# Optimization experiments

Hardware: AMD Instinct MI355X
Metric: run time of the kernel (lower is better)

The kernel has to match this reference:

```python
import jax, jax.numpy as jnp
import numpy as np

TOP_K = 2

def setup_inputs() -> dict:
    key = jax.random.key(0)
    k1, k2 = jax.random.split(key)
    B, S, D, E = 4, 8192, 1024, 64
    hidden_states = jax.random.normal(k1, (B, S, D), dtype=jnp.float32)
    gate_weight = jax.random.normal(k2, (E, D), dtype=jnp.float32) * (1.0 / D ** 0.5)
    return {"hidden_states": hidden_states, "gate_weight": gate_weight}

def reference(hidden_states, gate_weight):
    # router_logits: [B, S, E] = hidden @ W^T
    router_logits = jnp.einsum('bsd,ed->bse', hidden_states, gate_weight)
    # softmax in float32 (matches .float() in torch), cast back to input dtype
    router_probs = jax.nn.softmax(router_logits.astype(jnp.float32), axis=-1).astype(hidden_states.dtype)
    top_k_probs, selected_experts = jax.lax.top_k(router_probs, TOP_K)
    top_k_probs = top_k_probs / (jnp.sum(top_k_probs, axis=-1, keepdims=True) + 1e-08)
    return top_k_probs, selected_experts, router_logits
```

## Files before the change

### kernel.cpp

```cpp
#include <hip/hip_runtime.h>
#include <math.h>


typedef __attribute__((ext_vector_type(8))) short bf16x8;
typedef __attribute__((ext_vector_type(4))) float f32x4;

static constexpr int TOKENS = 32768;
static constexpr int DDIM   = 1024;
static constexpr int NEXP   = 64;
static constexpr size_t OFF_EXP = 65536;
static constexpr size_t OFF_LOG = 131072;

__global__ void w_split3_kernel(const float* __restrict__ w,
                                short* __restrict__ w1,
                                short* __restrict__ w2,
                                short* __restrict__ w3) {
    int idx = blockIdx.x * blockDim.x + threadIdx.x;
    for (int i = idx; i < NEXP * DDIM; i += gridDim.x * blockDim.x) {
        int e = i >> 10, k = i & 1023;
        float f = w[i];
        unsigned u1 = __float_as_uint(f);
        float f1 = __uint_as_float(u1 & 0xffff0000u);
        float r1 = f - f1;
        unsigned u2 = __float_as_uint(r1);
        float f2 = __uint_as_float(u2 & 0xffff0000u);
        float r2 = r1 - f2;
        unsigned u3 = __float_as_uint(r2);
        int n = e >> 4, c = k >> 5;
        int lane = (e & 15) + ((k & 31) >> 3) * 16;
        int j = k & 7;
        size_t dst = ((size_t)(c * 4 + n) * 64 + lane) * 8 + j;
        w1[dst] = (short)(u1 >> 16);
        w2[dst] = (short)(u2 >> 16);
        w3[dst] = (short)(u3 >> 16);
    }
}

__device__ inline void split8(float4 a, float4 b,
                              bf16x8& o1, bf16x8& o2, bf16x8& o3) {
    float f[8] = {a.x, a.y, a.z, a.w, b.x, b.y, b.z, b.w};
#pragma unroll
    for (int j = 0; j < 8; ++j) {
        unsigned u1 = __float_as_uint(f[j]);
        float f1 = __uint_as_float(u1 & 0xffff0000u);
        float r1 = f[j] - f1;
        unsigned u2 = __float_as_uint(r1);
        float f2 = __uint_as_float(u2 & 0xffff0000u);
        float r2 = r1 - f2;
        o1[j] = (short)(u1 >> 16);
        o2[j] = (short)(u2 >> 16);
        o3[j] = (short)(__float_as_uint(r2) >> 16);
    }
}

typedef const __attribute__((address_space(1))) unsigned int* gas1_t;
typedef __attribute__((address_space(3))) unsigned int* las3_t;
__device__ inline void stage16(const void* g, void* l) {
    __builtin_amdgcn_global_load_lds((gas1_t)(uintptr_t)g,
                                     (las3_t)(uintptr_t)l, 16, 0, 0);
}

__global__ __launch_bounds__(512, 4)
void router_mfma_kernel(const float* __restrict__ h,
                        const short* __restrict__ w1,
                        const short* __restrict__ w2,
                        const short* __restrict__ w3,
                        float* __restrict__ out) {
    __shared__ alignas(16) char smem[49152];
    const int tid   = threadIdx.x;
    const int lane  = tid & 63;
    const int wv    = tid >> 6;
    const int token0 = blockIdx.x * 128 + wv * 16;
    const int arow  = lane & 15;
    const int ks    = lane >> 4;

    const float* ap = h + (size_t)(token0 + arow) * DDIM + ks * 8;

    const short* warr[3] = {w1, w2, w3};
    const char* gsrc[3];
    int ldso[3];
#pragma unroll
    for (int i = 0; i < 3; ++i) {
        int seg = wv * 3 + i;
        int kc = seg / 12;
        int rem = seg % 12;
        int a = rem >> 2, n = rem & 3;
        gsrc[i] = (const char*)warr[a] + (size_t)kc * 65536 + n * 1024 + lane * 16;
        ldso[i] = (kc * 12 + a * 4 + n) * 1024;
    }

#define STAGE(bb, tt)                                                      \
    {                                                                      \
        _Pragma("unroll")                                                  \
        for (int i = 0; i < 3; ++i)                                        \
            stage16(gsrc[i] + (size_t)(tt) * 4096,                         \
                    smem + (bb) * 24576 + ldso[i]);                        \
    }

    f32x4 accA[4], accB[4];
#pragma unroll
    for (int n = 0; n < 4; ++n)
#pragma unroll
        for (int r = 0; r < 4; ++r) { accA[n][r] = 0.0f; accB[n][r] = 0.0f; }

    float4 ring[2][2][2];

    STAGE(0, 0);
    ring[0][0][0] = *reinterpret_cast<const float4*>(ap);
    ring[0][0][1] = *reinterpret_cast<const float4*>(ap + 4);
    ring[0][1][0] = *reinterpret_cast<const float4*>(ap + 512);
    ring[0][1][1] = *reinterpret_cast<const float4*>(ap + 516);
    asm volatile("s_waitcnt vmcnt(4)" ::: "memory");
    __builtin_amdgcn_s_barrier();

#pragma unroll
    for (int t = 0; t < 16; ++t) {
        const int b = t & 1;
        if (t + 1 < 16) {
            STAGE(b ^ 1, t + 1);
            ring[b ^ 1][0][0] =
                *reinterpret_cast<const float4*>(ap + (t + 1) * 32);
            ring[b ^ 1][0][1] =
                *reinterpret_cast<const float4*>(ap + (t + 1) * 32 + 4);
            ring[b ^ 1][1][0] =
                *reinterpret_cast<const float4*>(ap + 512 + (t + 1) * 32);
            ring[b ^ 1][1][1] =
                *reinterpret_cast<const float4*>(ap + 512 + (t + 1) * 32 + 4);
        }

        bf16x8 A1a, A2a, A3a, A1b, A2b, A3b;
        split8(ring[b][0][0], ring[b][0][1], A1a, A2a, A3a);
        split8(ring[b][1][0], ring[b][1][1], A1b, A2b, A3b);

        const char* wb0 = smem + b * 24576 + lane * 16;
        const char* wb1 = wb0 + 12288;
#pragma unroll
        for (int n = 0; n < 4; ++n) {
            bf16x8 W1v = *reinterpret_cast<const bf16x8*>(wb0 + n * 1024);
            bf16x8 W2v = *reinterpret_cast<const bf16x8*>(wb0 + n * 1024 + 4096);
            bf16x8 W3v = *reinterpret_cast<const bf16x8*>(wb0 + n * 1024 + 8192);
            f32x4 t0 = accA[n];
            t0 = __builtin_amdgcn_mfma_f32_16x16x32_bf16(A3a, W1v, t0, 0, 0, 0);
            t0 = __builtin_amdgcn_mfma_f32_16x16x32_bf16(A1a, W3v, t0, 0, 0, 0);
            t0 = __builtin_amdgcn_mfma_f32_16x16x32_bf16(A2a, W2v, t0, 0, 0, 0);
            t0 = __builtin_amdgcn_mfma_f32_16x16x32_bf16(A2a, W1v, t0, 0, 0, 0);
            t0 = __builtin_amdgcn_mfma_f32_16x16x32_bf16(A1a, W2v, t0, 0, 0, 0);
            t0 = __builtin_amdgcn_mfma_f32_16x16x32_bf16(A1a, W1v, t0, 0, 0, 0);
            accA[n] = t0;
            bf16x8 X1v = *reinterpret_cast<const bf16x8*>(wb1 + n * 1024);
            bf16x8 X2v = *reinterpret_cast<const bf16x8*>(wb1 + n * 1024 + 4096);
            bf16x8 X3v = *reinterpret_cast<const bf16x8*>(wb1 + n * 1024 + 8192);
            f32x4 t1 = accB[n];
            t1 = __builtin_amdgcn_mfma_f32_16x16x32_bf16(A3b, X1v, t1, 0, 0, 0);
            t1 = __builtin_amdgcn_mfma_f32_16x16x32_bf16(A1b, X3v, t1, 0, 0, 0);
            t1 = __builtin_amdgcn_mfma_f32_16x16x32_bf16(A2b, X2v, t1, 0, 0, 0);
            t1 = __builtin_amdgcn_mfma_f32_16x16x32_bf16(A2b, X1v, t1, 0, 0, 0);
            t1 = __builtin_amdgcn_mfma_f32_16x16x32_bf16(A1b, X2v, t1, 0, 0, 0);
            t1 = __builtin_amdgcn_mfma_f32_16x16x32_bf16(A1b, X1v, t1, 0, 0, 0);
            accB[n] = t1;
        }

        if (t + 1 < 16) {
            asm volatile("s_waitcnt vmcnt(4)" ::: "memory");
            __builtin_amdgcn_s_barrier();
        }
    }

    f32x4 acc[4];
#pragma unroll
    for (int n = 0; n < 4; ++n)
#pragma unroll
        for (int r = 0; r < 4; ++r) acc[n][r] = accA[n][r] + accB[n][r];

    const int rbase = (lane >> 4) * 4;
    const int col   = lane & 15;

#pragma unroll
    for (int n = 0; n < 4; ++n)
#pragma unroll
        for (int r = 0; r < 4; ++r)
            out[OFF_LOG + (size_t)(token0 + rbase + r) * NEXP + n * 16 + col]
                = acc[n][r];

#pragma unroll
    for (int r = 0; r < 4; ++r) {
        const int token = token0 + rbase + r;
        float mx = fmaxf(fmaxf(acc[0][r], acc[1][r]),
                         fmaxf(acc[2][r], acc[3][r]));
#pragma unroll
        for (int d = 1; d <= 8; d <<= 1) mx = fmaxf(mx, __shfl_xor(mx, d, 64));

        float p[4];
        float s = 0.0f;
#pragma unroll
        for (int n = 0; n < 4; ++n) { p[n] = expf(acc[n][r] - mx); s += p[n]; }
#pragma unroll
        for (int d = 1; d <= 8; d <<= 1) s += __shfl_xor(s, d, 64);

        float v1 = -INFINITY, v2 = -INFINITY;
        int   i1 = NEXP,      i2 = NEXP;
#pragma unroll
        for (int n = 0; n < 4; ++n) {
            float v = p[n];
            int   ei = n * 16 + col;
            if (v > v1)      { v2 = v1; i2 = i1; v1 = v; i1 = ei; }
            else if (v > v2) { v2 = v;  i2 = ei; }
        }

#pragma unroll
        for (int d = 1; d <= 8; d <<= 1) {
            float ov1 = __shfl_xor(v1, d, 64);
            float ov2 = __shfl_xor(v2, d, 64);
            int   oi1 = __shfl_xor(i1, d, 64);
            int   oi2 = __shfl_xor(i2, d, 64);
            bool ofirst = (ov1 > v1) || (ov1 == v1 && oi1 < i1);
            float n1, n2; int ni1, ni2;
            if (ofirst) {
                n1 = ov1; ni1 = oi1;
                bool sec = (v1 > ov2) || (v1 == ov2 && i1 < oi2);
                n2 = sec ? v1 : ov2; ni2 = sec ? i1 : oi2;
            } else {
                n1 = v1; ni1 = i1;
                bool sec = (ov1 > v2) || (ov1 == v2 && oi1 < i2);
                n2 = sec ? ov1 : v2; ni2 = sec ? oi1 : i2;
            }
            v1 = n1; i1 = ni1; v2 = n2; i2 = ni2;
        }

        if (col == 0) {
            float t1 = v1 / s;
            float t2 = v2 / s;
            float dn = t1 + t2 + 1e-8f;
            float2 pr; pr.x = t1 / dn; pr.y = t2 / dn;
            *reinterpret_cast<float2*>(out + (size_t)token * 2) = pr;
            float2 ex; ex.x = (float)i1; ex.y = (float)i2;
            *reinterpret_cast<float2*>(out + OFF_EXP + (size_t)token * 2) = ex;
        }
    }
#undef STAGE
}

extern "C" void kernel_launch(void* const* d_in, const int* in_sizes, int n_in,
                              void* d_out, int out_size, void* d_ws, size_t ws_size,
                              hipStream_t stream) {
    const float* h = (const float*)d_in[0];
    const float* w = (const float*)d_in[1];
    float* out = (float*)d_out;
    short* w1 = (short*)d_ws;
    short* w2 = w1 + (size_t)NEXP * DDIM;
    short* w3 = w2 + (size_t)NEXP * DDIM;
    hipLaunchKernelGGL(w_split3_kernel, dim3(128), dim3(256), 0, stream, w, w1, w2, w3);
    hipLaunchKernelGGL(router_mfma_kernel, dim3(TOKENS / 128), dim3(512), 0, stream,
                       h, w1, w2, w3, out);
}
```

Before: 47.09 us.

## Switch router GEMM to 32x32x16 MFMA with split-K across wave pairs

Replaces the 16x16x32 bf16 MFMA tiling with 32x32x16 MFMAs. Each wave pair now covers 32 tokens, and the two waves split the K dimension into halves, reducing their partial sums through LDS before the softmax/top-k epilogue. The weight pre-split layout is changed to match the 32x32 operand lane mapping. The intent is to get higher MFMA throughput per instruction and fewer LDS weight reads per FLOP. In exchange it adds an LDS reduction with extra barriers, idles half the waves during the epilogue, and widens the shuffle reductions to 32 lanes.

```diff
diff --git a/kernel.cpp b/kernel.cpp
--- a/kernel.cpp
+++ b/kernel.cpp
@@ -2,8 +2,8 @@
 #include <math.h>
 
 
-typedef __attribute__((ext_vector_type(8))) short bf16x8;
-typedef __attribute__((ext_vector_type(4))) float f32x4;
+typedef __attribute__((ext_vector_type(8)))  short bf16x8;
+typedef __attribute__((ext_vector_type(16))) float f32x16;
 
 static constexpr int TOKENS = 32768;
 static constexpr int DDIM   = 1024;
@@ -26,10 +26,11 @@
         float f2 = __uint_as_float(u2 & 0xffff0000u);
         float r2 = r1 - f2;
         unsigned u3 = __float_as_uint(r2);
-        int n = e >> 4, c = k >> 5;
-        int lane = (e & 15) + ((k & 31) >> 3) * 16;
+        int nt = e >> 5, col = e & 31;
+        int kstep = k >> 4;
+        int lane = col + 32 * ((k >> 3) & 1);
         int j = k & 7;
-        size_t dst = ((size_t)(c * 4 + n) * 64 + lane) * 8 + j;
+        size_t dst = ((size_t)(kstep * 2 + nt) * 64 + lane) * 8 + j;
         w1[dst] = (short)(u1 >> 16);
         w2[dst] = (short)(u2 >> 16);
         w3[dst] = (short)(u3 >> 16);
@@ -67,14 +68,16 @@
                         const short* __restrict__ w3,
                         float* __restrict__ out) {
     __shared__ alignas(16) char smem[49152];
-    const int tid   = threadIdx.x;
-    const int lane  = tid & 63;
-    const int wv    = tid >> 6;
-    const int token0 = blockIdx.x * 128 + wv * 16;
-    const int arow  = lane & 15;
-    const int ks    = lane >> 4;
-
-    const float* ap = h + (size_t)(token0 + arow) * DDIM + ks * 8;
+    const int tid  = threadIdx.x;
+    const int lane = tid & 63;
+    const int wv   = tid >> 6;
+    const int kh   = wv & 1;
+    const int mg   = wv >> 1;
+    const int token0 = blockIdx.x * 128 + mg * 32;
+    const int col  = lane & 31;
+    const int hh   = lane >> 5;
+
+    const float* ap = h + (size_t)(token0 + col) * DDIM + kh * 512 + hh * 8;
 
     const short* warr[3] = {w1, w2, w3};
     const char* gsrc[3];
@@ -82,11 +85,12 @@
 #pragma unroll
     for (int i = 0; i < 3; ++i) {
         int seg = wv * 3 + i;
-        int kc = seg / 12;
-        int rem = seg % 12;
-        int a = rem >> 2, n = rem & 3;
-        gsrc[i] = (const char*)warr[a] + (size_t)kc * 65536 + n * 1024 + lane * 16;
-        ldso[i] = (kc * 12 + a * 4 + n) * 1024;
+        int kh_s = seg / 12;
+        int rem  = seg % 12;
+        int arr  = rem >> 2, q = rem & 3;
+        gsrc[i] = (const char*)warr[arr] + (size_t)kh_s * 65536 + q * 1024
+                + lane * 16;
+        ldso[i] = kh_s * 12288 + arr * 4096 + q * 1024;
     }
 
 #define STAGE(bb, tt)                                                      \
@@ -97,19 +101,19 @@
                     smem + (bb) * 24576 + ldso[i]);                        \
     }
 
-    f32x4 accA[4], accB[4];
-#pragma unroll
-    for (int n = 0; n < 4; ++n)
-#pragma unroll
-        for (int r = 0; r < 4; ++r) { accA[n][r] = 0.0f; accB[n][r] = 0.0f; }
+    f32x16 acc[2];
+#pragma unroll
+    for (int nt = 0; nt < 2; ++nt)
+#pragma unroll
+        for (int q = 0; q < 16; ++q) acc[nt][q] = 0.0f;
 
     float4 ring[2][2][2];
 
     STAGE(0, 0);
     ring[0][0][0] = *reinterpret_cast<const float4*>(ap);
     ring[0][0][1] = *reinterpret_cast<const float4*>(ap + 4);
-    ring[0][1][0] = *reinterpret_cast<const float4*>(ap + 512);
-    ring[0][1][1] = *reinterpret_cast<const float4*>(ap + 516);
+    ring[0][1][0] = *reinterpret_cast<const float4*>(ap + 16);
+    ring[0][1][1] = *reinterpret_cast<const float4*>(ap + 20);
     asm volatile("s_waitcnt vmcnt(4)" ::: "memory");
     __builtin_amdgcn_s_barrier();
 
@@ -123,42 +127,33 @@
             ring[b ^ 1][0][1] =
                 *reinterpret_cast<const float4*>(ap + (t + 1) * 32 + 4);
             ring[b ^ 1][1][0] =
-                *reinterpret_cast<const float4*>(ap + 512 + (t + 1) * 32);
+                *reinterpret_cast<const float4*>(ap + (t + 1) * 32 + 16);
             ring[b ^ 1][1][1] =
-                *reinterpret_cast<const float4*>(ap + 512 + (t + 1) * 32 + 4);
-        }
-
-        bf16x8 A1a, A2a, A3a, A1b, A2b, A3b;
-        split8(ring[b][0][0], ring[b][0][1], A1a, A2a, A3a);
-        split8(ring[b][1][0], ring[b][1][1], A1b, A2b, A3b);
-
-        const char* wb0 = smem + b * 24576 + lane * 16;
-        const char* wb1 = wb0 + 12288;
-#pragma unroll
-        for (int n = 0; n < 4; ++n) {
-            bf16x8 W1v = *reinterpret_cast<const bf16x8*>(wb0 + n * 1024);
-            bf16x8 W2v = *reinterpret_cast<const bf16x8*>(wb0 + n * 1024 + 4096);
-            bf16x8 W3v = *reinterpret_cast<const bf16x8*>(wb0 + n * 1024 + 8192);
-            f32x4 t0 = accA[n];
-            t0 = __builtin_amdgcn_mfma_f32_16x16x32_bf16(A3a, W1v, t0, 0, 0, 0);
-            t0 = __builtin_amdgcn_mfma_f32_16x16x32_bf16(A1a, W3v, t0, 0, 0, 0);
-            t0 = __builtin_amdgcn_mfma_f32_16x16x32_bf16(A2a, W2v, t0, 0, 0, 0);
-            t0 = __builtin_amdgcn_mfma_f32_16x16x32_bf16(A2a, W1v, t0, 0, 0, 0);
-            t0 = __builtin_amdgcn_mfma_f32_16x16x32_bf16(A1a, W2v, t0, 0, 0, 0);
-            t0 = __builtin_amdgcn_mfma_f32_16x16x32_bf16(A1a, W1v, t0, 0, 0, 0);
-            accA[n] = t0;
-            bf16x8 X1v = *reinterpret_cast<const bf16x8*>(wb1 + n * 1024);
-            bf16x8 X2v = *reinterpret_cast<const bf16x8*>(wb1 + n * 1024 + 4096);
-            bf16x8 X3v = *reinterpret_cast<const bf16x8*>(wb1 + n * 1024 + 8192);
-            f32x4 t1 = accB[n];
-            t1 = __builtin_amdgcn_mfma_f32_16x16x32_bf16(A3b, X1v, t1, 0, 0, 0);
-            t1 = __builtin_amdgcn_mfma_f32_16x16x32_bf16(A1b, X3v, t1, 0, 0, 0);
-            t1 = __builtin_amdgcn_mfma_f32_16x16x32_bf16(A2b, X2v, t1, 0, 0, 0);
-            t1 = __builtin_amdgcn_mfma_f32_16x16x32_bf16(A2b, X1v, t1, 0, 0, 0);
-            t1 = __builtin_amdgcn_mfma_f32_16x16x32_bf16(A1b, X2v, t1, 0, 0, 0);
-            t1 = __builtin_amdgcn_mfma_f32_16x16x32_bf16(A1b, X1v, t1, 0, 0, 0);
-            accB[n] = t1;
-        }
+                *reinterpret_cast<const float4*>(ap + (t + 1) * 32 + 20);
+        }
+
+        bf16x8 A1[2], A2[2], A3[2];
+        split8(ring[b][0][0], ring[b][0][1], A1[0], A2[0], A3[0]);
+        split8(ring[b][1][0], ring[b][1][1], A1[1], A2[1], A3[1]);
+
+        const char* wb = smem + b * 24576 + kh * 12288 + lane * 16;
+#pragma unroll
+        for (int si = 0; si < 2; ++si)
+#pragma unroll
+            for (int nt = 0; nt < 2; ++nt) {
+                const int q = si * 2 + nt;
+                bf16x8 W1v = *reinterpret_cast<const bf16x8*>(wb + q * 1024);
+                bf16x8 W2v = *reinterpret_cast<const bf16x8*>(wb + q * 1024 + 4096);
+                bf16x8 W3v = *reinterpret_cast<const bf16x8*>(wb + q * 1024 + 8192);
+                f32x16 t2 = acc[nt];
+                t2 = __builtin_amdgcn_mfma_f32_32x32x16_bf16(A3[si], W1v, t2, 0, 0, 0);
+                t2 = __builtin_amdgcn_mfma_f32_32x32x16_bf16(A1[si], W3v, t2, 0, 0, 0);
+                t2 = __builtin_amdgcn_mfma_f32_32x32x16_bf16(A2[si], W2v, t2, 0, 0, 0);
+                t2 = __builtin_amdgcn_mfma_f32_32x32x16_bf16(A2[si], W1v, t2, 0, 0, 0);
+                t2 = __builtin_amdgcn_mfma_f32_32x32x16_bf16(A1[si], W2v, t2, 0, 0, 0);
+                t2 = __builtin_amdgcn_mfma_f32_32x32x16_bf16(A1[si], W1v, t2, 0, 0, 0);
+                acc[nt] = t2;
+            }
 
         if (t + 1 < 16) {
             asm volatile("s_waitcnt vmcnt(4)" ::: "memory");
@@ -166,49 +161,54 @@
         }
     }
 
-    f32x4 acc[4];
-#pragma unroll
-    for (int n = 0; n < 4; ++n)
-#pragma unroll
-        for (int r = 0; r < 4; ++r) acc[n][r] = accA[n][r] + accB[n][r];
-
-    const int rbase = (lane >> 4) * 4;
-    const int col   = lane & 15;
-
-#pragma unroll
-    for (int n = 0; n < 4; ++n)
-#pragma unroll
-        for (int r = 0; r < 4; ++r)
-            out[OFF_LOG + (size_t)(token0 + rbase + r) * NEXP + n * 16 + col]
-                = acc[n][r];
-
-#pragma unroll
-    for (int r = 0; r < 4; ++r) {
-        const int token = token0 + rbase + r;
-        float mx = fmaxf(fmaxf(acc[0][r], acc[1][r]),
-                         fmaxf(acc[2][r], acc[3][r]));
-#pragma unroll
-        for (int d = 1; d <= 8; d <<= 1) mx = fmaxf(mx, __shfl_xor(mx, d, 64));
-
-        float p[4];
-        float s = 0.0f;
-#pragma unroll
-        for (int n = 0; n < 4; ++n) { p[n] = expf(acc[n][r] - mx); s += p[n]; }
-#pragma unroll
-        for (int d = 1; d <= 8; d <<= 1) s += __shfl_xor(s, d, 64);
-
-        float v1 = -INFINITY, v2 = -INFINITY;
-        int   i1 = NEXP,      i2 = NEXP;
-#pragma unroll
-        for (int n = 0; n < 4; ++n) {
-            float v = p[n];
-            int   ei = n * 16 + col;
-            if (v > v1)      { v2 = v1; i2 = i1; v1 = v; i1 = ei; }
-            else if (v > v2) { v2 = v;  i2 = ei; }
-        }
-
-#pragma unroll
-        for (int d = 1; d <= 8; d <<= 1) {
+    __syncthreads();
+
+    if (kh == 1) {
+        float* cA = (float*)smem + (size_t)(mg * 64 + lane) * 33;
+#pragma unroll
+        for (int nt = 0; nt < 2; ++nt)
+#pragma unroll
+            for (int q = 0; q < 16; ++q) cA[nt * 16 + q] = acc[nt][q];
+    }
+    __syncthreads();
+    if (kh != 0) return;
+
+    {
+        const float* cA = (const float*)smem + (size_t)(mg * 64 + lane) * 33;
+#pragma unroll
+        for (int nt = 0; nt < 2; ++nt)
+#pragma unroll
+            for (int q = 0; q < 16; ++q) acc[nt][q] += cA[nt * 16 + q];
+    }
+
+#pragma unroll
+    for (int q = 0; q < 16; ++q) {
+        const int row = (q & 3) + 8 * (q >> 2) + 4 * hh;
+        float* lg = out + OFF_LOG + (size_t)(token0 + row) * NEXP + col;
+        lg[0]  = acc[0][q];
+        lg[32] = acc[1][q];
+    }
+
+#pragma unroll
+    for (int q = 0; q < 16; ++q) {
+        const int token = token0 + (q & 3) + 8 * (q >> 2) + 4 * hh;
+        float p0v = acc[0][q], p1v = acc[1][q];
+        float mx = fmaxf(p0v, p1v);
+#pragma unroll
+        for (int d = 1; d <= 16; d <<= 1) mx = fmaxf(mx, __shfl_xor(mx, d, 64));
+
+        float e0 = expf(p0v - mx);
+        float e1 = expf(p1v - mx);
+        float s = e0 + e1;
+#pragma unroll
+        for (int d = 1; d <= 16; d <<= 1) s += __shfl_xor(s, d, 64);
+
+        float v1, v2; int i1, i2;
+        if (e1 > e0) { v1 = e1; i1 = 32 + col; v2 = e0; i2 = col; }
+        else         { v1 = e0; i1 = col;      v2 = e1; i2 = 32 + col; }
+
+#pragma unroll
+        for (int d = 1; d <= 16; d <<= 1) {
             float ov1 = __shfl_xor(v1, d, 64);
             float ov2 = __shfl_xor(v2, d, 64);
             int   oi1 = __shfl_xor(i1, d, 64);
```

Result: slower. 64.76 us (+37.5%).
